# Performance work log

Measured on AMD Instinct MI355X. Metric: run time of the kernel, lower is better.

## Reference

```python
import jax, jax.numpy as jnp
import numpy as np

N, E, IN_CH, HIDDEN, N_CLASS, LAYERS = 2048, 1024, 512, 512, 40, 10
EPS = 1e-10


def setup_inputs() -> dict:
    key = jax.random.key(0)
    ks = jax.random.split(key, 6)
    x = jax.random.normal(ks[0], (1, N, IN_CH), jnp.float32)
    H = (jax.random.uniform(ks[1], (N, E)) < 0.02).astype(jnp.float32)
    # symmetric Laplacian-like operator so eigh is meaningful
    M = jax.random.normal(ks[2], (1, N, N), jnp.float32) / np.sqrt(N).astype(np.float32)
    L = 0.5 * (M + jnp.swapaxes(M, 1, 2))
    W_first = jax.random.normal(ks[3], (HIDDEN, IN_CH), jnp.float32) * 0.05
    W_mid = jax.random.normal(ks[4], (LAYERS - 2, HIDDEN, HIDDEN), jnp.float32) * 0.05
    W_last = jax.random.normal(ks[5], (N_CLASS, HIDDEN), jnp.float32) * 0.05
    return {"x": x, "L": L, "H": H, "W_first": W_first, "W_mid": W_mid, "W_last": W_last}


def _expanded_energy(x2d, H, d_v, d_e):
    # Vectorized form of the nested hyperedge/pair loop:
    # sum_e sum_{u<v in e} H_ue*H_ve/(d_e+eps) * ||x_u/sqrt(dv_u+eps) - x_v/sqrt(dv_v+eps)||^2
    # = sum_e (s_e * q_e - ||m_e||^2) / (d_e + eps)  with binary H (w_e = 1)
    y = x2d / jnp.sqrt(d_v + EPS)[:, None]          # [N, F]
    q = H.T @ jnp.sum(y * y, axis=1)                # [E] sum_u H_ue ||y_u||^2
    m = H.T @ y                                     # [E, F]
    s = jnp.sum(H, axis=0)                          # [E] edge degrees (= d_e)
    return jnp.sum((s * q - jnp.sum(m * m, axis=1)) / (d_e + EPS))


def reference(x, L, H, W_first, W_mid, W_last):
    weights = [W_first] + [W_mid[i] for i in range(LAYERS - 2)] + [W_last]
    d_v = jnp.sum(H, axis=1)
    d_e = jnp.sum(H, axis=0)
    # eigh of L is identical every layer in the original; compute once
    eigvals = jnp.linalg.eigh(L)[0]                 # [B, N]
    spectral_gap = jnp.min(jnp.where(eigvals > 1e-10, eigvals, jnp.inf))
    energies, energies_exp, snorms = [], [], []
    for i, W in enumerate(weights):
        x = jax.nn.relu(jnp.einsum('bnm,bmf->bnf', L, x) @ W.T)
        xs, Ls = x[0], L[0]                         # @torch.no_grad() blocks
        energies.append(jnp.trace(xs.T @ (Ls @ xs)))
        energies_exp.append(_expanded_energy(xs, H, d_v, d_e))
        snorms.append(jnp.linalg.norm(W, ord=2))
        # dropout skipped (eval-mode reference)
    log_probs = jax.nn.log_softmax(x, axis=1)       # dim=1 as in original
    return (log_probs, jnp.stack(energies), jnp.stack(energies_exp),
            jnp.stack(snorms), spectral_gap)
```

## Files before the change

kernel.cpp:

```cpp
#include <hip/hip_runtime.h>
#include <math.h>


typedef __attribute__((ext_vector_type(8))) short short8;
typedef __attribute__((ext_vector_type(4))) float f32x4;

#define NSHIFT 256

__device__ inline ushort bf16_rne(float f) {
    unsigned int u = __float_as_uint(f);
    return (ushort)((u + 0x7FFFu + ((u >> 16) & 1u)) >> 16);
}
__device__ inline float bf16_tof(ushort h) {
    return __uint_as_float(((unsigned int)h) << 16);
}

__device__ __forceinline__ void pbar(int* bar, int e, int w, int nwg) {
    __syncthreads();
    if (threadIdx.x == 0) {
        __threadfence();
        __hip_atomic_store(bar + 16 + w*16, e, __ATOMIC_RELAXED, __HIP_MEMORY_SCOPE_AGENT);
    }
    if (w == 0) {
        if ((int)threadIdx.x < nwg) {
            while (__hip_atomic_load(bar + 16 + threadIdx.x*16, __ATOMIC_RELAXED,
                                     __HIP_MEMORY_SCOPE_AGENT) < e)
                __builtin_amdgcn_s_sleep(1);
        }
        __syncthreads();
        if (threadIdx.x == 0)
            __hip_atomic_store(bar, e, __ATOMIC_RELEASE, __HIP_MEMORY_SCOPE_AGENT);
    } else {
        if (threadIdx.x == 0) {
            while (__hip_atomic_load(bar, __ATOMIC_RELAXED, __HIP_MEMORY_SCOPE_AGENT) < e)
                __builtin_amdgcn_s_sleep(8);
        }
    }
    if (threadIdx.x == 0) __threadfence();
    __syncthreads();
}

__global__ void init_misc(int* bar) {
    for (int j = blockIdx.x*256 + threadIdx.x; j < 16384; j += gridDim.x*256) bar[j] = 0;
}

template<bool TA, bool TB>
__device__ __forceinline__
void tile64g(const float* __restrict__ A, int lda,
             const float* __restrict__ B, int ldb,
             int bm, int bn, int k0, int k1, float acc[4][4],
             float (*sA)[68], float (*sB)[68])
{
    const int tid = threadIdx.x;
    const int tx = tid & 15, ty = tid >> 4;
    for (int kk = k0; kk < k1; kk += 16) {
        __syncthreads();
        for (int i = tid; i < 1024; i += 256) {
            int m, k2;
            if (TA) { m = i & 63; k2 = i >> 6; } else { k2 = i & 15; m = i >> 4; }
            sA[k2][m] = TA ? A[(size_t)(kk + k2)*lda + bm + m]
                           : A[(size_t)(bm + m)*lda + kk + k2];
        }
        for (int i = tid; i < 1024; i += 256) {
            int n, k2;
            if (TB) { k2 = i & 15; n = i >> 4; } else { n = i & 63; k2 = i >> 6; }
            sB[k2][n] = TB ? B[(size_t)(bn + n)*ldb + kk + k2]
                           : B[(size_t)(kk + k2)*ldb + bn + n];
        }
        __syncthreads();
        #pragma unroll
        for (int k2 = 0; k2 < 16; ++k2) {
            float4 a4 = *(const float4*)&sA[k2][ty*4];
            float4 b4 = *(const float4*)&sB[k2][tx*4];
            float av[4] = {a4.x, a4.y, a4.z, a4.w};
            float bv[4] = {b4.x, b4.y, b4.z, b4.w};
            #pragma unroll
            for (int i2 = 0; i2 < 4; ++i2)
                #pragma unroll
                for (int j2 = 0; j2 < 4; ++j2)
                    acc[i2][j2] += av[i2] * bv[j2];
        }
    }
}

template<bool TA, bool TB>
__device__ __forceinline__
void tile64d(const float* __restrict__ A, int lda,
             const float* __restrict__ B, int ldb,
             int bm, int bn, int k0, int k1, float acc[4][4],
             float (*sA)[16][68], float (*sB)[16][68])
{
    const int tid = threadIdx.x;
    const int tx = tid & 15, ty = tid >> 4;
    float ra[4], rb[4];
    auto ldregs = [&](int kk) {
        #pragma unroll
        for (int q = 0; q < 4; ++q) {
            int i = tid + q*256;
            if (TA) { int m = i & 63, k2 = i >> 6; ra[q] = A[(size_t)(kk + k2)*lda + bm + m]; }
            else    { int k2 = i & 15, m = i >> 4; ra[q] = A[(size_t)(bm + m)*lda + kk + k2]; }
            if (TB) { int k3 = i & 15, n = i >> 4; rb[q] = B[(size_t)(bn + n)*ldb + kk + k3]; }
            else    { int k3 = i >> 6, n = i & 63; rb[q] = B[(size_t)(kk + k3)*ldb + bn + n]; }
        }
    };
    auto stlds = [&](int buf) {
        #pragma unroll
        for (int q = 0; q < 4; ++q) {
            int i = tid + q*256;
            if (TA) { int m = i & 63, k2 = i >> 6; sA[buf][k2][m] = ra[q]; }
            else    { int k2 = i & 15, m = i >> 4; sA[buf][k2][m] = ra[q]; }
            if (TB) { int k3 = i & 15, n = i >> 4; sB[buf][k3][n] = rb[q]; }
            else    { int k3 = i >> 6, n = i & 63; sB[buf][k3][n] = rb[q]; }
        }
    };
    const int nit = (k1 - k0) >> 4;
    ldregs(k0);
    stlds(0);
    for (int it = 0; it < nit; ++it) {
        const int buf = it & 1;
        if (it + 1 < nit) ldregs(k0 + (it + 1)*16);
        __syncthreads();
        #pragma unroll
        for (int k2 = 0; k2 < 16; ++k2) {
            float4 a4 = *(const float4*)&sA[buf][k2][ty*4];
            float4 b4 = *(const float4*)&sB[buf][k2][tx*4];
            float av[4] = {a4.x, a4.y, a4.z, a4.w};
            float bv[4] = {b4.x, b4.y, b4.z, b4.w};
            #pragma unroll
            for (int i2 = 0; i2 < 4; ++i2)
                #pragma unroll
                for (int j2 = 0; j2 < 4; ++j2)
                    acc[i2][j2] += av[i2] * bv[j2];
        }
        if (it + 1 < nit) { __syncthreads(); stlds(buf ^ 1); }
    }
}

__device__ __forceinline__ void store_tile(float* C, int ldc, int bm, float acc[4][4]) {
    int tx = threadIdx.x & 15, ty = threadIdx.x >> 4;
    #pragma unroll
    for (int i = 0; i < 4; ++i)
        #pragma unroll
        for (int j = 0; j < 4; ++j)
            C[(size_t)(bm + ty*4 + i)*ldc + tx*4 + j] = acc[i][j];
}

__global__ void init_q0(float* Q) {
    int idx = blockIdx.x*256 + threadIdx.x;
    if (idx < 2048*64) {
        int n = idx >> 6, c = idx & 63;
        Q[(size_t)n*2048 + c] = (n == c) ? 1.f : 0.f;
    }
}

__global__ __launch_bounds__(256)
void lz_LQ(const float* __restrict__ Lm, const float* __restrict__ Qs, float* __restrict__ Cp)
{
    __shared__ float sA[2][16][68], sB[2][16][68];
    int z = blockIdx.x, mt = blockIdx.y;
    float acc[4][4] = {};
    tile64d<false,false>(Lm, 2048, Qs, 2048, mt*64, 0, z*256, z*256 + 256, acc, sA, sB);
    store_tile(Cp + (size_t)z*131072, 64, mt*64, acc);
}

__global__ void lz_sumZ(const float* __restrict__ Cp, float* __restrict__ Z)
{
    int idx = blockIdx.x*256 + threadIdx.x;
    float v = 0.f;
    #pragma unroll
    for (int z = 0; z < 8; ++z) v += Cp[(size_t)z*131072 + idx];
    Z[idx] = v;
}

__global__ __launch_bounds__(256)
void lz_QTZ(const float* __restrict__ Qall, const float* __restrict__ Z, float* __restrict__ Cp)
{
    __shared__ float sA[2][16][68], sB[2][16][68];
    int z = blockIdx.x, b = blockIdx.y;
    float acc[4][4] = {};
    tile64d<true,false>(Qall, 2048, Z, 64, b*64, 0, z*256, z*256 + 256, acc, sA, sB);
    store_tile(Cp + (size_t)z*131072, 64, b*64, acc);
}

__global__ void lz_sumC(const float* __restrict__ Cp, float* __restrict__ Creo,
                        float* __restrict__ Ab, int s)
{
    int idx = blockIdx.x*256 + threadIdx.x;
    float v = 0.f;
    #pragma unroll
    for (int z = 0; z < 8; ++z) v += Cp[(size_t)z*131072 + idx];
    Creo[idx] = v;
    if ((idx >> 6) >= 64*s) Ab[(size_t)s*4096 + (idx - s*4096)] = v;
}

__global__ __launch_bounds__(256)
void lz_QC(const float* __restrict__ Qall, const float* __restrict__ Creo,
           float* __restrict__ Cp, int s)
{
    __shared__ float sA[2][16][68], sB[2][16][68];
    int z = blockIdx.x, mt = blockIdx.y;
    float acc[4][4] = {};
    for (int j = z; j <= s; j += 8)
        tile64d<false,false>(Qall, 2048, Creo, 64, mt*64, 0, j*64, j*64 + 64, acc, sA, sB);
    store_tile(Cp + (size_t)z*131072, 64, mt*64, acc);
}

__global__ __launch_bounds__(256)
void lz_finZ(float* __restrict__ Z, const float* __restrict__ Cp, int nz,
             double* __restrict__ Gp)
{
    __shared__ float zb[64][65];
    int w = blockIdx.x, tid = threadIdx.x;
    for (int idx = tid; idx < 4096; idx += 256) {
        size_t o = (size_t)w*4096 + idx;
        float v = Z[o];
        for (int z = 0; z < nz; ++z) v -= Cp[(size_t)z*131072 + o];
        Z[o] = v;
        zb[idx >> 6][idx & 63] = v;
    }
    __syncthreads();
    int tx = tid & 15, ty = tid >> 4;
    double acc[4][4] = {};
    for (int r = 0; r < 64; ++r) {
        float av[4], bv[4];
        #pragma unroll
        for (int q = 0; q < 4; ++q) { av[q] = zb[r][ty*4 + q]; bv[q] = zb[r][tx*4 + q]; }
        #pragma unroll
        for (int i = 0; i < 4; ++i)
            #pragma unroll
            for (int j = 0; j < 4; ++j)
                acc[i][j] += (double)av[i] * (double)bv[j];
    }
    #pragma unroll
    for (int i = 0; i < 4; ++i)
        #pragma unroll
        for (int j = 0; j < 4; ++j)
            Gp[(size_t)w*4096 + (size_t)(ty*4 + i)*64 + tx*4 + j] = acc[i][j];
}

__global__ __launch_bounds__(256)
void lz_chol(const double* __restrict__ Gp, float* __restrict__ RinvF, float* __restrict__ BbS)
{
    __shared__ double G[64][65];
    __shared__ double Xs[64][65];
    __shared__ double lv[64];
    int tid = threadIdx.x;
    for (int idx = tid; idx < 4096; idx += 256) {
        double g = 0.0;
        for (int z = 0; z < 32; ++z) g += Gp[(size_t)z*4096 + idx];
        G[idx>>6][idx&63] = g;
    }
    __syncthreads();
    for (int k = 0; k < 64; ++k) {
        if (tid < 64) {
            double rkk = sqrt(fmax(G[k][k], 1e-40));
            lv[tid] = (tid == k) ? rkk : ((tid > k) ? G[k][tid]/rkk : 0.0);
        }
        __syncthreads();
        if (tid < 64 && tid >= k) G[k][tid] = lv[tid];
        for (int idx = tid; idx < 4096; idx += 256) {
            int i = idx>>6, j = idx&63;
            if (i > k && j >= i) G[i][j] -= lv[i]*lv[j];
        }
        __syncthreads();
    }
    for (int idx = tid; idx < 4096; idx += 256) {
        int i = idx>>6, j = idx&63;
        BbS[idx] = (j >= i) ? (float)G[i][j] : 0.f;
        Xs[i][j] = 0.0;
    }
    __syncthreads();
    if (tid < 64) {
        int j = tid;
        for (int i = j; i >= 0; --i) {
            double s2 = (i == j) ? 1.0 : 0.0;
            for (int k2 = i + 1; k2 <= j; ++k2) s2 -= G[i][k2]*Xs[k2][j];
            Xs[i][j] = s2 / G[i][i];
        }
    }
    __syncthreads();
    for (int idx = tid; idx < 4096; idx += 256)
        RinvF[idx] = (float)Xs[idx>>6][idx&63];
}

__global__ __launch_bounds__(256)
void lz_apply(const float* __restrict__ Z, const float* __restrict__ Rinv, float* __restrict__ Qn)
{
    __shared__ float sA[2][16][68], sB[2][16][68];
    int w = blockIdx.x;
    float acc[4][4] = {};
    tile64d<false,false>(Z, 64, Rinv, 64, w*64, 0, 0, 64, acc, sA, sB);
    store_tile(Qn, 2048, w*64, acc);
}

__global__ void assemble_band(const float* Ab, const float* Bb, float* band) {
    int idx = blockIdx.x*256 + threadIdx.x;
    if (idx >= 2048*65) return;
    int c = idx / 65, r = idx % 65;
    int row = c + r;
    float v = 0.f;
    if (row < 2048) {
        int j = c >> 6, q = c & 63, rr = q + r;
        if (rr <= 63) {
            const float* A = Ab + (size_t)j*4096;
            v = 0.5f*(A[rr*64 + q] + A[q*64 + rr]);
        } else if (j < 31) {
            int p = rr - 64;
            v = Bb[(size_t)j*4096 + p*64 + q];
        }
    }
    band[idx] = v;
}

__device__ __forceinline__
void pack_item(int idx, const float* __restrict__ src, const float* __restrict__ dv,
               ushort* __restrict__ Bh, ushort* __restrict__ Bl,
               ushort* __restrict__ Ch, ushort* __restrict__ Cl)
{
    int l = idx & 63, t = idx >> 6;
    int nb = t & 31, kc = t >> 5;
    int col = nb*16 + (l & 15);
    int k0 = kc*32 + ((l >> 4) << 3);
    ushort h8[8], l8[8], sh8[8], sl8[8];
    #pragma unroll
    for (int j = 0; j < 8; ++j) {
        int k = k0 + j;
        float v = src[(size_t)k*512 + col];
        ushort hb = bf16_rne(v);
        h8[j] = hb; l8[j] = bf16_rne(v - bf16_tof(hb));
        if (Ch) {
            float t2 = v * (1.0f / sqrtf(dv[k] + 1e-10f));
            ushort hb2 = bf16_rne(t2);
            sh8[j] = hb2; sl8[j] = bf16_rne(t2 - bf16_tof(hb2));
        }
    }
    uint4 hv, lv;
    hv.x = (unsigned)h8[0] | ((unsigned)h8[1] << 16);
    hv.y = (unsigned)h8[2] | ((unsigned)h8[3] << 16);
    hv.z = (unsigned)h8[4] | ((unsigned)h8[5] << 16);
    hv.w = (unsigned)h8[6] | ((unsigned)h8[7] << 16);
    lv.x = (unsigned)l8[0] | ((unsigned)l8[1] << 16);
    lv.y = (unsigned)l8[2] | ((unsigned)l8[3] << 16);
    lv.z = (unsigned)l8[4] | ((unsigned)l8[5] << 16);
    lv.w = (unsigned)l8[6] | ((unsigned)l8[7] << 16);
    *(uint4*)(Bh + (size_t)idx*8) = hv;
    *(uint4*)(Bl + (size_t)idx*8) = lv;
    if (Ch) {
        uint4 shv, slv;
        shv.x = (unsigned)sh8[0] | ((unsigned)sh8[1] << 16);
        shv.y = (unsigned)sh8[2] | ((unsigned)sh8[3] << 16);
        shv.z = (unsigned)sh8[4] | ((unsigned)sh8[5] << 16);
        shv.w = (unsigned)sh8[6] | ((unsigned)sh8[7] << 16);
        slv.x = (unsigned)sl8[0] | ((unsigned)sl8[1] << 16);
        slv.y = (unsigned)sl8[2] | ((unsigned)sl8[3] << 16);
        slv.z = (unsigned)sl8[4] | ((unsigned)sl8[5] << 16);
        slv.w = (unsigned)sl8[6] | ((unsigned)sl8[7] << 16);
        *(uint4*)(Ch + (size_t)idx*8) = shv;
        *(uint4*)(Cl + (size_t)idx*8) = slv;
    }
}

__global__ void pack_both(const float* __restrict__ src, const float* __restrict__ dv,
                          ushort* __restrict__ Bh, ushort* __restrict__ Bl,
                          ushort* __restrict__ Ch, ushort* __restrict__ Cl)
{
    int idx = blockIdx.x*256 + threadIdx.x;
    if (idx < 131072) pack_item(idx, src, dv, Bh, Bl, Ch, Cl);
}

__global__ void pack_A_L(const float* __restrict__ src, int Kld, int MB,
                         ushort* __restrict__ Ah, ushort* __restrict__ Al, int total)
{
    int idx = blockIdx.x*256 + threadIdx.x;
    if (idx >= total) return;
    int l = idx & 63, t = idx >> 6;
    int mb = t % MB, kc = t / MB;
    int m = mb*16 + (l & 15);
    int k0 = kc*32 + ((l >> 4) << 3);
    const float* p = src + (size_t)m*Kld + k0;
    float4 a = *(const float4*)p, b = *(const float4*)(p + 4);
    float vv[8] = {a.x,a.y,a.z,a.w,b.x,b.y,b.z,b.w};
    ushort h8[8], l8[8];
    #pragma unroll
    for (int j = 0; j < 8; ++j) {
        ushort hb = bf16_rne(vv[j]);
        h8[j] = hb; l8[j] = bf16_rne(vv[j] - bf16_tof(hb));
    }
    uint4 hv, lv;
    hv.x = (unsigned)h8[0] | ((unsigned)h8[1] << 16);
    hv.y = (unsigned)h8[2] | ((unsigned)h8[3] << 16);
    hv.z = (unsigned)h8[4] | ((unsigned)h8[5] << 16);
    hv.w = (unsigned)h8[6] | ((unsigned)h8[7] << 16);
    lv.x = (unsigned)l8[0] | ((unsigned)l8[1] << 16);
    lv.y = (unsigned)l8[2] | ((unsigned)l8[3] << 16);
    lv.z = (unsigned)l8[4] | ((unsigned)l8[5] << 16);
    lv.w = (unsigned)l8[6] | ((unsigned)l8[7] << 16);
    *(uint4*)(Ah + (size_t)idx*8) = hv;
    *(uint4*)(Al + (size_t)idx*8) = lv;
}

__global__ void pack_A_T(const float* __restrict__ src, int Mld, int MB,
                         ushort* __restrict__ Ah, int total)
{
    int idx = blockIdx.x*256 + threadIdx.x;
    if (idx >= total) return;
    int l = idx & 63, t = idx >> 6;
    int mb = t % MB, kc = t / MB;
    int m = mb*16 + (l & 15);
    int k0 = kc*32 + ((l >> 4) << 3);
    ushort h8[8];
    #pragma unroll
    for (int j = 0; j < 8; ++j)
        h8[j] = bf16_rne(src[(size_t)(k0 + j)*Mld + m]);
    uint4 hv;
    hv.x = (unsigned)h8[0] | ((unsigned)h8[1] << 16);
    hv.y = (unsigned)h8[2] | ((unsigned)h8[3] << 16);
    hv.z = (unsigned)h8[4] | ((unsigned)h8[5] << 16);
    hv.w = (unsigned)h8[6] | ((unsigned)h8[7] << 16);
    *(uint4*)(Ah + (size_t)idx*8) = hv;
}

__device__ __forceinline__
void mfma_task(int t, const ushort* __restrict__ Lph, const ushort* __restrict__ Lpl,
               const ushort* __restrict__ Bh, const ushort* __restrict__ Bl,
               const ushort* __restrict__ Htp,
               const ushort* __restrict__ Bqh, const ushort* __restrict__ Bql,
               float* __restrict__ U, float* __restrict__ ME,
               ushort (*lA)[4096], ushort (*lB)[4096])
{
    const bool isU = (t < 64);
    const ushort* Ah = isU ? Lph : Htp;
    const ushort* Al = isU ? Lpl : nullptr;
    const ushort* Xh = isU ? Bh : Bqh;
    const ushort* Xl = isU ? Bl : Bql;
    float* C = isU ? U : ME;
    const int MB = isU ? 128 : 64;
    const int tmb = (isU ? (t >> 2) : ((t - 64) >> 2)) * 8;
    const int tnb = (t & 3) * 8;
    const int KC = 64;
    const int tid = threadIdx.x;
    const int lane = tid & 63, wave = tid >> 6;
    const int wr = wave >> 1, wc = wave & 1;

    f32x4 acc[4][4];
    #pragma unroll
    for (int i = 0; i < 4; ++i)
        #pragma unroll
        for (int j = 0; j < 4; ++j) acc[i][j] = (f32x4){0.f,0.f,0.f,0.f};

    uint4 rAh[2], rAl[2], rBh[2], rBl[2];
    auto loadregs = [&](int kc) {
        const uint4* pa = (const uint4*)(Ah + ((size_t)kc*MB + tmb)*512);
        rAh[0] = pa[tid]; rAh[1] = pa[tid + 256];
        if (Al) {
            const uint4* pl = (const uint4*)(Al + ((size_t)kc*MB + tmb)*512);
            rAl[0] = pl[tid]; rAl[1] = pl[tid + 256];
        }
        const uint4* pb = (const uint4*)(Xh + ((size_t)kc*32 + tnb)*512);
        rBh[0] = pb[tid]; rBh[1] = pb[tid + 256];
        const uint4* pc = (const uint4*)(Xl + ((size_t)kc*32 + tnb)*512);
        rBl[0] = pc[tid]; rBl[1] = pc[tid + 256];
    };

    loadregs(0);
    for (int kc = 0; kc < KC; ++kc) {
        __syncthreads();
        *(uint4*)&lA[0][tid*8]       = rAh[0];
        *(uint4*)&lA[0][(tid+256)*8] = rAh[1];
        if (Al) {
            *(uint4*)&lA[1][tid*8]       = rAl[0];
            *(uint4*)&lA[1][(tid+256)*8] = rAl[1];
        }
        *(uint4*)&lB[0][tid*8]       = rBh[0];
        *(uint4*)&lB[0][(tid+256)*8] = rBh[1];
        *(uint4*)&lB[1][tid*8]       = rBl[0];
        *(uint4*)&lB[1][(tid+256)*8] = rBl[1];
        if (kc + 1 < KC) loadregs(kc + 1);
        __syncthreads();

        short8 a_h[4], a_l[4], b_h[4], b_l[4];
        #pragma unroll
        for (int i = 0; i < 4; ++i) {
            a_h[i] = *(const short8*)&lA[0][(((wr*4 + i)*64) + lane)*8];
            if (Al) a_l[i] = *(const short8*)&lA[1][(((wr*4 + i)*64) + lane)*8];
        }
        #pragma unroll
        for (int j = 0; j < 4; ++j) {
            b_h[j] = *(const short8*)&lB[0][(((wc*4 + j)*64) + lane)*8];
            b_l[j] = *(const short8*)&lB[1][(((wc*4 + j)*64) + lane)*8];
        }
        #pragma unroll
        for (int i = 0; i < 4; ++i)
            #pragma unroll
            for (int j = 0; j < 4; ++j) {
                acc[i][j] = __builtin_amdgcn_mfma_f32_16x16x32_bf16(a_h[i], b_h[j], acc[i][j], 0, 0, 0);
                acc[i][j] = __builtin_amdgcn_mfma_f32_16x16x32_bf16(a_h[i], b_l[j], acc[i][j], 0, 0, 0);
                if (Al)
                    acc[i][j] = __builtin_amdgcn_mfma_f32_16x16x32_bf16(a_l[i], b_h[j], acc[i][j], 0, 0, 0);
            }
    }
    const int r0 = tmb*16 + wr*64, c0 = tnb*16 + wc*64;
    #pragma unroll
    for (int i = 0; i < 4; ++i)
        #pragma unroll
        for (int j = 0; j < 4; ++j) {
            int row = r0 + i*16 + ((lane >> 4) << 2);
            int col = c0 + j*16 + (lane & 15);
            #pragma unroll
            for (int r = 0; r < 4; ++r)
                C[(size_t)(row + r)*512 + col] = acc[i][j][r];
        }
}

__global__ __launch_bounds__(256, 2)
void mgemm_dual(const ushort* __restrict__ Lph, const ushort* __restrict__ Lpl,
                const ushort* __restrict__ Bh, const ushort* __restrict__ Bl,
                const ushort* __restrict__ Htp,
                const ushort* __restrict__ Bqh, const ushort* __restrict__ Bql,
                float* __restrict__ U, float* __restrict__ ME)
{
    __shared__ ushort lA[2][4096];
    __shared__ ushort lB[2][4096];
    int t = blockIdx.y * 4 + blockIdx.x;
    mfma_task(t, Lph, Lpl, Bh, Bl, Htp, Bqh, Bql, U, ME, lA, lB);
}

__global__ __launch_bounds__(256, 1)
void mlp_persist(float* __restrict__ u, float* __restrict__ h,
                 const float* __restrict__ Wf, const float* __restrict__ Wm,
                 const ushort* __restrict__ Lph, const ushort* __restrict__ Lpl,
                 const ushort* __restrict__ Htp,
                 ushort* __restrict__ bpkh, ushort* __restrict__ bpkl,
                 ushort* __restrict__ bqh, ushort* __restrict__ bql,
                 const float* __restrict__ H, const float* __restrict__ dv,
                 const float* __restrict__ de,
                 float* __restrict__ mEb, float* __restrict__ srowp,
                 float* __restrict__ qpart,
                 float* __restrict__ parts512, float* __restrict__ parts16,
                 float* __restrict__ outp, int* __restrict__ bar)
{
    const int w = blockIdx.x, tid = threadIdx.x;
    __shared__ char smem[35072];
    __shared__ float red4[4];
    __shared__ float sRs[64];
    float (*sA)[68] = (float(*)[68])smem;
    float (*sB)[68] = (float(*)[68])(smem + 4352);
    float (*sT)[65] = (float(*)[65])smem;
    ushort (*lA)[4096] = (ushort(*)[4096])smem;
    ushort (*lB)[4096] = (ushort(*)[4096])(smem + 16384);
    int ep = 0;
    const int mt = w >> 3, nt = w & 7;
    const int tx = tid & 15, ty = tid >> 4;

    for (int k = 0; k < 9; ++k) {
        const float* W = (k == 0) ? Wf : Wm + (size_t)(k-1)*262144;
        if (w == 0 && k > 0 && tid < 64) {
            float s = parts512[tid] + parts512[tid+64] + parts512[tid+128] + parts512[tid+192];
            for (int o = 32; o; o >>= 1) s += __shfl_down(s, o, 64);
            float x = (tid < 16) ? parts16[tid] : 0.f;
            for (int o = 32; o; o >>= 1) x += __shfl_down(x, o, 64);
            if (tid == 0) { outp[81920 + k - 1] = s; outp[81930 + k - 1] = x; }
        }
        {
            float acc[4][4] = {};
            tile64g<false,true>(u, 512, W, 512, mt*64, nt*64, 0, 512, acc, sA, sB);
            __syncthreads();
            if (tid < 64) sRs[tid] = 1.0f / sqrtf(dv[mt*64 + tid] + 1e-10f);
            #pragma unroll
            for (int i = 0; i < 4; ++i)
                #pragma unroll
                for (int j = 0; j < 4; ++j) {
                    float v = fmaxf(acc[i][j], 0.f);
                    h[(size_t)(mt*64 + ty*4 + i)*512 + nt*64 + tx*4 + j] = v;
                    sT[ty*4 + i][tx*4 + j] = v;
                }
            __syncthreads();
            #pragma unroll
            for (int q = 0; q < 2; ++q) {
                int it = tid + q*256;
                int a = it >> 8, rem = it & 255;
                int b = rem >> 6, lane = rem & 63;
                int cl = b*16 + (lane & 15);
                int r0 = a*32 + ((lane >> 4) << 3);
                int idxg = (((2*mt + a)*32 + (4*nt + b))*64 + lane);
                ushort h8[8], l8[8], sh8[8], sl8[8];
                #pragma unroll
                for (int j = 0; j < 8; ++j) {
                    float v = sT[r0 + j][cl];
                    ushort hb = bf16_rne(v);
                    h8[j] = hb; l8[j] = bf16_rne(v - bf16_tof(hb));
                    float t2 = v * sRs[r0 + j];
                    ushort hb2 = bf16_rne(t2);
                    sh8[j] = hb2; sl8[j] = bf16_rne(t2 - bf16_tof(hb2));
                }
                uint4 hv, lv, shv, slv;
                hv.x = (unsigned)h8[0] | ((unsigned)h8[1] << 16);
                hv.y = (unsigned)h8[2] | ((unsigned)h8[3] << 16);
                hv.z = (unsigned)h8[4] | ((unsigned)h8[5] << 16);
                hv.w = (unsigned)h8[6] | ((unsigned)h8[7] << 16);
                lv.x = (unsigned)l8[0] | ((unsigned)l8[1] << 16);
                lv.y = (unsigned)l8[2] | ((unsigned)l8[3] << 16);
                lv.z = (unsigned)l8[4] | ((unsigned)l8[5] << 16);
                lv.w = (unsigned)l8[6] | ((unsigned)l8[7] << 16);
                shv.x = (unsigned)sh8[0] | ((unsigned)sh8[1] << 16);
                shv.y = (unsigned)sh8[2] | ((unsigned)sh8[3] << 16);
                shv.z = (unsigned)sh8[4] | ((unsigned)sh8[5] << 16);
                shv.w = (unsigned)sh8[6] | ((unsigned)sh8[7] << 16);
                slv.x = (unsigned)sl8[0] | ((unsigned)sl8[1] << 16);
                slv.y = (unsigned)sl8[2] | ((unsigned)sl8[3] << 16);
                slv.z = (unsigned)sl8[4] | ((unsigned)sl8[5] << 16);
                slv.w = (unsigned)sl8[6] | ((unsigned)sl8[7] << 16);
                *(uint4*)(bpkh + (size_t)idxg*8) = hv;
                *(uint4*)(bpkl + (size_t)idxg*8) = lv;
                *(uint4*)(bqh  + (size_t)idxg*8) = shv;
                *(uint4*)(bql  + (size_t)idxg*8) = slv;
            }
            if (tid < 64) {
                float rs = sRs[tid];
                float ss = 0.f;
                for (int c = 0; c < 64; ++c) { float v = sT[tid][c]; ss += v*v; }
                srowp[(size_t)nt*2048 + mt*64 + tid] = ss * rs * rs;
            }
        }
        pbar(bar, ++ep, w, 256);
        if (w < 96) {
            mfma_task(w, Lph, Lpl, bpkh, bpkl, Htp, bqh, bql, u, mEb, lA, lB);
        } else if (w < 128) {
            int task = w - 96;
            int e = (task & 3)*256 + tid;
            int zc = task >> 2;
            float s = 0.f;
            for (int n = zc*256; n < zc*256 + 256; ++n) {
                float sr = 0.f;
                #pragma unroll
                for (int p2 = 0; p2 < 8; ++p2) sr += srowp[(size_t)p2*2048 + n];
                s += H[(size_t)n*1024 + e] * sr;
            }
            qpart[(size_t)zc*1024 + e] = s;
        }
        pbar(bar, ++ep, w, 256);
        if (w < 16) {
            int wave = tid >> 6, lane = tid & 63;
            float acc = 0.f;
            for (int t2 = 0; t2 < 16; ++t2) {
                int e = w*64 + wave*16 + t2;
                float me2 = 0.f;
                for (int f = lane; f < 512; f += 64) { float v = mEb[(size_t)e*512 + f]; me2 += v*v; }
                for (int o = 32; o; o >>= 1) me2 += __shfl_down(me2, o, 64);
                if (lane == 0) {
                    float q = 0.f;
                    for (int z = 0; z < 8; ++z) q += qpart[(size_t)z*1024 + e];
                    acc += (de[e]*q - me2) / (de[e] + 1e-10f);
                }
            }
            if (lane == 0) red4[wave] = acc;
            __syncthreads();
            if (tid == 0) parts16[w] = red4[0]+red4[1]+red4[2]+red4[3];
            __syncthreads();
        }
        {
            int lane = tid & 63;
            float dd = 0.f;
            #pragma unroll
            for (int g = 0; g < 2; ++g) {
                int row = w*8 + g*4 + (tid >> 6);
                for (int f = lane; f < 512; f += 64)
                    dd += h[(size_t)row*512 + f] * u[(size_t)row*512 + f];
            }
            for (int o = 32; o; o >>= 1) dd += __shfl_down(dd, o, 64);
            __syncthreads();
            if (lane == 0) red4[tid >> 6] = dd;
            __syncthreads();
            if (tid == 0) parts512[w] = red4[0]+red4[1]+red4[2]+red4[3];
        }
        pbar(bar, ++ep, w, 256);
    }
    if (w == 0 && tid < 64) {
        float s = parts512[tid] + parts512[tid+64] + parts512[tid+128] + parts512[tid+192];
        for (int o = 32; o; o >>= 1) s += __shfl_down(s, o, 64);
        float x = (tid < 16) ? parts16[tid] : 0.f;
        for (int o = 32; o; o >>= 1) x += __shfl_down(x, o, 64);
        if (tid == 0) { outp[81928] = s; outp[81938] = x; }
    }
}

template<bool TA, bool TB>
__global__ __launch_bounds__(256)
void gemm_f32(const float* A, int lda, const float* B, int ldb,
              float* C, int ldc, float* Cpart,
              int M, int N, int K, float alpha, float beta, int relu)
{
    const int S = (int)gridDim.z, z = (int)blockIdx.z;
    const int kchunk = (K + S - 1) / S;
    const int k0 = z * kchunk;
    const int k1 = (K < k0 + kchunk) ? K : (k0 + kchunk);
    const int bm = blockIdx.y * 64, bn = blockIdx.x * 64;
    __shared__ float As[16][68];
    __shared__ float Bs[16][68];
    const int tid = threadIdx.x;
    const int tx = tid & 15, ty = tid >> 4;
    float acc[4][4] = {};
    for (int kk = k0; kk < k1; kk += 16) {
        for (int i = tid; i < 1024; i += 256) {
            int m, k;
            if (TA) { m = i & 63; k = i >> 6; } else { k = i & 15; m = i >> 4; }
            int gm = bm + m, gk = kk + k;
            float v = 0.f;
            if (gm < M && gk < k1) v = TA ? A[(size_t)gk*lda + gm] : A[(size_t)gm*lda + gk];
            As[k][m] = v;
        }
        for (int i = tid; i < 1024; i += 256) {
            int n, k;
            if (TB) { k = i & 15; n = i >> 4; } else { n = i & 63; k = i >> 6; }
            int gn = bn + n, gk = kk + k;
            float v = 0.f;
            if (gn < N && gk < k1) v = TB ? B[(size_t)gn*ldb + gk] : B[(size_t)gk*ldb + gn];
            Bs[k][n] = v;
        }
        __syncthreads();
        #pragma unroll
        for (int k = 0; k < 16; ++k) {
            float4 ra4 = *reinterpret_cast<const float4*>(&As[k][ty*4]);
            float4 rb4 = *reinterpret_cast<const float4*>(&Bs[k][tx*4]);
            float ra[4] = {ra4.x, ra4.y, ra4.z, ra4.w};
            float rb[4] = {rb4.x, rb4.y, rb4.z, rb4.w};
            #pragma unroll
            for (int i = 0; i < 4; ++i)
                #pragma unroll
                for (int j = 0; j < 4; ++j)
                    acc[i][j] += ra[i] * rb[j];
        }
        __syncthreads();
    }
    if (S == 1) {
        #pragma unroll
        for (int i = 0; i < 4; ++i) {
            int gm = bm + ty*4 + i;
            if (gm >= M) continue;
            #pragma unroll
            for (int j = 0; j < 4; ++j) {
                int gn = bn + tx*4 + j;
                if (gn >= N) continue;
                float v = alpha * acc[i][j];
                if (beta != 0.f) v += beta * C[(size_t)gm*ldc + gn];
                if (relu) v = fmaxf(v, 0.f);
                C[(size_t)gm*ldc + gn] = v;
            }
        }
    } else {
        float* P = Cpart + (size_t)z * M * N;
        #pragma unroll
        for (int i = 0; i < 4; ++i) {
            int gm = bm + ty*4 + i;
            if (gm >= M) continue;
            #pragma unroll
            for (int j = 0; j < 4; ++j) {
                int gn = bn + tx*4 + j;
                if (gn >= N) continue;
                P[(size_t)gm*N + gn] = alpha * acc[i][j];
            }
        }
    }
}

__global__ void reduce_parts(const float* Cpart, float* C, int M, int N, int ldc,
                             int S, float beta, int relu)
{
    int total = M * N;
    for (int idx = blockIdx.x*256 + threadIdx.x; idx < total; idx += gridDim.x*256) {
        float s = 0.f;
        for (int z = 0; z < S; ++z) s += Cpart[(size_t)z*total + idx];
        int mm = idx / N, nn = idx % N;
        float v = s;
        if (beta != 0.f) v += beta * C[(size_t)mm*ldc + nn];
        if (relu) v = fmaxf(v, 0.f);
        C[(size_t)mm*ldc + nn] = v;
    }
}

__global__ void row_deg(const float* H, float* dv) {
    int row = blockIdx.x*4 + (threadIdx.x >> 6);
    int lane = threadIdx.x & 63;
    if (row >= 2048) return;
    float s = 0.f;
    for (int e = lane; e < 1024; e += 64) s += H[(size_t)row*1024 + e];
    for (int o = 32; o; o >>= 1) s += __shfl_down(s, o, 64);
    if (lane == 0) dv[row] = s;
}

__global__ void coldot_part(const float* H, const float* w, float* part) {
    int e = blockIdx.x*256 + threadIdx.x;
    int zc = blockIdx.y;
    float s = 0.f;
    if (w) {
        for (int n = zc*256; n < zc*256 + 256; ++n) s += H[(size_t)n*1024 + e] * w[n];
    } else {
        for (int n = zc*256; n < zc*256 + 256; ++n) s += H[(size_t)n*1024 + e];
    }
    part[(size_t)zc*1024 + e] = s;
}
__global__ void coldot_fin(const float* part, float* outp) {
    int e = blockIdx.x*256 + threadIdx.x;
    float s = 0.f;
    for (int z = 0; z < 8; ++z) s += part[(size_t)z*1024 + e];
    outp[e] = s;
}

__global__ void dotsrow(const float* h, const float* u, int F, const float* dv,
                        float* srow, float* yout, float* parts)
{
    int row = blockIdx.x*4 + (threadIdx.x >> 6);
    int lane = threadIdx.x & 63;
    __shared__ float a4[4];
    float rs = 1.0f / sqrtf(dv[row] + 1e-10f);
    float ss = 0.f, dd = 0.f;
    for (int f = lane; f < F; f += 64) {
        float hv = h[(size_t)row*F + f];
        float t = hv * rs;
        if (yout) yout[(size_t)row*F + f] = t;
        ss += t*t;
        dd += hv * u[(size_t)row*F + f];
    }
    for (int o = 32; o; o >>= 1) { ss += __shfl_down(ss, o, 64); dd += __shfl_down(dd, o, 64); }
    if (lane == 0) { srow[row] = ss; a4[threadIdx.x >> 6] = dd; }
    __syncthreads();
    if (threadIdx.x == 0) parts[blockIdx.x] = a4[0]+a4[1]+a4[2]+a4[3];
}

__global__ void edge_energy(const float* m, int F, const float* de, const float* qpart,
                            float* partials) {
    int wave = threadIdx.x >> 6, lane = threadIdx.x & 63;
    __shared__ float acc4[4];
    float acc = 0.f;
    for (int t = 0; t < 16; ++t) {
        int e = blockIdx.x*64 + wave*16 + t;
        float me2 = 0.f;
        for (int f = lane; f < F; f += 64) { float v = m[(size_t)e*F + f]; me2 += v*v; }
        for (int o = 32; o; o >>= 1) me2 += __shfl_down(me2, o, 64);
        if (lane == 0) {
            float q = 0.f;
            for (int z = 0; z < 8; ++z) q += qpart[(size_t)z*1024 + e];
            acc += (de[e]*q - me2) / (de[e] + 1e-10f);
        }
    }
    if (lane == 0) acc4[wave] = acc;
    __syncthreads();
    if (threadIdx.x == 0) partials[blockIdx.x] = acc4[0]+acc4[1]+acc4[2]+acc4[3];
}

__global__ void finalize2(const float* p512, const float* p16, float* oe, float* ox) {
    __shared__ float red[256];
    int tid = threadIdx.x;
    red[tid] = p512[tid] + p512[tid + 256];
    __syncthreads();
    for (int st = 128; st; st >>= 1) { if (tid < st) red[tid] += red[tid+st]; __syncthreads(); }
    if (tid == 0) *oe = red[0];
    __syncthreads();
    red[tid] = (tid < 16) ? p16[tid] : 0.f;
    __syncthreads();
    for (int st = 128; st; st >>= 1) { if (tid < st) red[tid] += red[tid+st]; __syncthreads(); }
    if (tid == 0) *ox = red[0];
}

__global__ void logsoftmax(const float* xf, float* outp) {
    __shared__ float red[256];
    int c = blockIdx.x, tid = threadIdx.x;
    float mx = -3.0e38f;
    for (int n = tid; n < 2048; n += 256) mx = fmaxf(mx, xf[(size_t)n*40 + c]);
    red[tid] = mx; __syncthreads();
    for (int st = 128; st; st >>= 1) { if (tid < st) red[tid] = fmaxf(red[tid], red[tid+st]); __syncthreads(); }
    mx = red[0]; __syncthreads();
    float s = 0.f;
    for (int n = tid; n < 2048; n += 256) s += expf(xf[(size_t)n*40 + c] - mx);
    red[tid] = s; __syncthreads();
    for (int st = 128; st; st >>= 1) { if (tid < st) red[tid] += red[tid+st]; __syncthreads(); }
    float lse = mx + logf(red[0]);
    for (int n = tid; n < 2048; n += 256) outp[(size_t)n*40 + c] = xf[(size_t)n*40 + c] - lse;
}

__global__ __launch_bounds__(256)
void band_count(const float* __restrict__ band, const double* __restrict__ shifts,
                int* __restrict__ counts)
{
    __shared__ double win[66][66];
    const int tid = threadIdx.x;
    const double sigma = shifts[blockIdx.x];
    int ei[9], ej[9];
    {
        int i = 1, S = 0;
        #pragma unroll
        for (int k = 0; k < 9; ++k) {
            int T = tid + k*256;
            if (T < 2080) {
                while (S + (65 - i) <= T) { S += 65 - i; ++i; }
                ei[k] = i; ej[k] = i + (T - S);
            } else { ei[k] = 0; ej[k] = 0; }
        }
    }
    for (int idx = tid; idx < 65*65; idx += 256) {
        int c0 = idx / 65, r = idx % 65;
        win[c0][r] = (double)band[c0*65 + r] - (r == 0 ? sigma : 0.0);
    }
    __syncthreads();
    int cnt = 0;
    for (int c = 0; c < 2048; ++c) {
        const int p = c % 66;
        double d = win[p][0];
        if (fabs(d) < 1e-100) d = (d < 0 ? -1e-100 : 1e-100);
        if (d < 0) cnt++;
        double inv = 1.0 / d;
        #pragma unroll
        for (int k = 0; k < 9; ++k) {
            int i = ei[k];
            if (i) {
                int j = ej[k];
                int r2 = p + i; if (r2 >= 66) r2 -= 66;
                win[r2][j - i] -= win[p][i] * inv * win[p][j];
            }
        }
        int cn = c + 65;
        int slot = p + 65; if (slot >= 66) slot -= 66;
        if (tid < 65)
            win[slot][tid] = (cn < 2048)
                ? ((double)band[(size_t)cn*65 + tid] - (tid == 0 ? sigma : 0.0)) : 0.0;
        __syncthreads();
    }
    if (tid == 0) counts[blockIdx.x] = cnt;
}

__global__ void bisect(double* shifts, const int* counts, double* st, float* gap_out, int mode) {
    if (threadIdx.x != 0) return;
    if (mode == 0) {
        shifts[0] = 1e-10;
        double l0 = log(1e-6), l1 = log(0.5);
        for (int i = 1; i < NSHIFT; ++i) shifts[i] = exp(l0 + (l1 - l0)*(i - 1)/(double)(NSHIFT - 2));
        return;
    }
    if (mode == 1) {
        int n0 = counts[0];
        double lo = shifts[NSHIFT-1], hi = 1.5;
        for (int i = 1; i < NSHIFT; ++i) if (counts[i] > n0) { lo = shifts[i-1]; hi = shifts[i]; break; }
        st[0] = lo; st[1] = hi; st[2] = (double)n0;
        for (int i = 0; i < NSHIFT; ++i) shifts[i] = lo + (hi - lo)*(i + 1)/(double)(NSHIFT + 1);
        return;
    }
    int n0 = (int)st[2];
    double lo = st[0], hi = st[1];
    double nlo = shifts[NSHIFT-1], nhi = hi;
    for (int i = 0; i < NSHIFT; ++i) if (counts[i] > n0) { nhi = shifts[i]; nlo = (i == 0) ? lo : shifts[i-1]; break; }
    *gap_out = (float)(0.5*(nlo + nhi));
}

__global__ __launch_bounds__(256)
void gram9(const float* __restrict__ Wf, const float* __restrict__ Wm, float* __restrict__ sG)
{
    int mi = blockIdx.z;
    const float* W = (mi == 0) ? Wf : Wm + (size_t)(mi-1)*262144;
    __shared__ float sA[16][68], sB[16][68];
    int tid = threadIdx.x, tx = tid & 15, ty = tid >> 4;
    int bm = blockIdx.y*64, bn = blockIdx.x*64;
    float acc[4][4] = {};
    for (int kk = 0; kk < 512; kk += 16) {
        __syncthreads();
        for (int i = tid; i < 1024; i += 256) { int m = i&63, k = i>>6; sA[k][m] = W[(size_t)(kk+k)*512 + bm+m]; }
        for (int i = tid; i < 1024; i += 256) { int n = i&63, k = i>>6; sB[k][n] = W[(size_t)(kk+k)*512 + bn+n]; }
        __syncthreads();
        #pragma unroll
        for (int k = 0; k < 16; ++k) {
            float4 a4 = *(const float4*)&sA[k][ty*4];
            float4 b4 = *(const float4*)&sB[k][tx*4];
            float av[4]={a4.x,a4.y,a4.z,a4.w}, bv[4]={b4.x,b4.y,b4.z,b4.w};
            #pragma unroll
            for (int i = 0; i < 4; ++i)
                #pragma unroll
                for (int j = 0; j < 4; ++j) acc[i][j] += av[i]*bv[j];
        }
    }
    float* C = sG + (size_t)mi*262144;
    #pragma unroll
    for (int i = 0; i < 4; ++i)
        #pragma unroll
        for (int j = 0; j < 4; ++j)
            C[(size_t)(bm + ty*4 + i)*512 + bn + tx*4 + j] = acc[i][j];
}

__global__ __launch_bounds__(256)
void snorm_lanczos(const float* Gall, const float* Wl, float* outp) {
    int w = blockIdx.x, tid = threadIdx.x;
    int n = (w < 9) ? 512 : 40;
    const float* G = Gall + (size_t)w*262144;
    __shared__ float g40[1600];
    __shared__ float v[512], vp[512], wv[512], red[256];
    __shared__ float al[32], be[32];
    if (w == 9) {
        for (int p = tid; p < 1600; p += 256) {
            int i = p / 40, j = p % 40;
            float s = 0.f;
            for (int k2 = 0; k2 < 512; ++k2) s += Wl[(size_t)i*512 + k2]*Wl[(size_t)j*512 + k2];
            g40[p] = s;
        }
        __syncthreads();
    }
    float inv0 = 1.f / sqrtf((float)n);
    for (int i = tid; i < n; i += 256) { v[i] = inv0; vp[i] = 0.f; }
    __syncthreads();
    float beta_prev = 0.f;
    for (int s = 0; s < 32; ++s) {
        for (int r = tid; r < n; r += 256) {
            float sum = 0.f;
            if (w < 9) { const float* row = G + (size_t)r*512; for (int k2 = 0; k2 < 512; ++k2) sum += row[k2]*v[k2]; }
            else       { const float* row = &g40[r*40];        for (int k2 = 0; k2 < 40;  ++k2) sum += row[k2]*v[k2]; }
            wv[r] = sum;
        }
        __syncthreads();
        float p = 0.f;
        for (int i = tid; i < n; i += 256) p += v[i]*wv[i];
        red[tid] = p; __syncthreads();
        for (int st = 128; st; st >>= 1) { if (tid < st) red[tid] += red[tid+st]; __syncthreads(); }
        float alpha = red[0]; __syncthreads();
        for (int i = tid; i < n; i += 256) wv[i] -= alpha*v[i] + beta_prev*vp[i];
        __syncthreads();
        p = 0.f;
        for (int i = tid; i < n; i += 256) p += wv[i]*wv[i];
        red[tid] = p; __syncthreads();
        for (int st = 128; st; st >>= 1) { if (tid < st) red[tid] += red[tid+st]; __syncthreads(); }
        float beta = sqrtf(fmaxf(red[0], 0.f)); __syncthreads();
        if (tid == 0) { al[s] = alpha; be[s] = beta; }
        float ib = 1.f / fmaxf(beta, 1e-20f);
        for (int i = tid; i < n; i += 256) { float t = v[i]; vp[i] = t; v[i] = wv[i]*ib; }
        beta_prev = beta;
        __syncthreads();
    }
    if (tid == 0) {
        float hi = 0.f;
        for (int s = 0; s < 32; ++s) {
            float g2 = al[s] + be[s] + (s ? be[s-1] : 0.f);
            hi = fmaxf(hi, g2);
        }
        float lo = 0.f;
        for (int it = 0; it < 48; ++it) {
            float mid = 0.5f*(lo + hi);
            float d = al[0] - mid; int c2 = (d < 0.f);
            for (int s = 1; s < 32; ++s) {
                float dp = d;
                if (fabsf(dp) < 1e-25f) dp = (dp < 0.f) ? -1e-25f : 1e-25f;
                d = (al[s] - mid) - be[s-1]*be[s-1]/dp;
                c2 += (d < 0.f);
            }
            if (c2 == 32) hi = mid; else lo = mid;
        }
        outp[w] = sqrtf(fmaxf(0.5f*(lo + hi), 0.f));
    }
}

static void gemm64(hipStream_t st, int ta, int tb, int M, int N, int K,
                   const float* A, int lda, const float* B, int ldb,
                   float* C, int ldc, float alpha, float beta, int relu,
                   float* Cpart, int S)
{
    dim3 grid((unsigned)((N + 63)/64), (unsigned)((M + 63)/64), (unsigned)S);
    if (!ta && !tb)      gemm_f32<false,false><<<grid,256,0,st>>>(A,lda,B,ldb,C,ldc,Cpart,M,N,K,alpha,beta,relu);
    else if (!ta && tb)  gemm_f32<false,true ><<<grid,256,0,st>>>(A,lda,B,ldb,C,ldc,Cpart,M,N,K,alpha,beta,relu);
    else if (ta && !tb)  gemm_f32<true ,false><<<grid,256,0,st>>>(A,lda,B,ldb,C,ldc,Cpart,M,N,K,alpha,beta,relu);
    else                 gemm_f32<true ,true ><<<grid,256,0,st>>>(A,lda,B,ldb,C,ldc,Cpart,M,N,K,alpha,beta,relu);
    if (S > 1) {
        int total = M * N;
        int g = (total + 255)/256; if (g > 2048) g = 2048;
        reduce_parts<<<g,256,0,st>>>(Cpart, C, M, N, ldc, S, beta, relu);
    }
}

extern "C" void kernel_launch(void* const* d_in, const int* in_sizes, int n_in,
                              void* d_out, int out_size, void* d_ws, size_t ws_size,
                              hipStream_t stream)
{
    (void)in_sizes; (void)n_in; (void)out_size; (void)ws_size;
    const float* X  = (const float*)d_in[0];
    const float* Lm = (const float*)d_in[1];
    const float* H  = (const float*)d_in[2];
    const float* Wf = (const float*)d_in[3];
    const float* Wm = (const float*)d_in[4];
    const float* Wl = (const float*)d_in[5];
    float* out = (float*)d_out;

    float* ws = (float*)d_ws;
    size_t off = 0;
    auto alloc = [&](size_t n) { float* p = ws + off; off += (n + 255) & ~(size_t)255; return p; };
    float* Lph_f  = alloc((size_t)2097152);
    float* Lpl_f  = alloc((size_t)2097152);
    float* Htp_f  = alloc((size_t)1048576);
    float* bpkh_f = alloc((size_t)524288);
    float* bpkl_f = alloc((size_t)524288);
    float* h      = alloc((size_t)2048*512);
    float* u      = alloc((size_t)2048*512);
    float* mEb    = alloc((size_t)1024*512);
    float* Cpart  = alloc((size_t)1024*1024);
    float* srowp  = alloc((size_t)8*2048);
    float* dv     = alloc(2048);
    float* de     = alloc(1024);
    float* srow   = alloc(2048);
    float* qpart  = alloc(8*1024);
    float* parts512 = alloc(512);
    float* parts16  = alloc(256);
    double* shifts  = (double*)alloc(2*NSHIFT);
    double* bstate  = (double*)alloc(8);
    int* counts     = (int*)alloc(NSHIFT);
    int* barbase    = (int*)alloc(16384);

    ushort* Lph  = (ushort*)Lph_f;
    ushort* Lpl  = (ushort*)Lpl_f;
    ushort* Htp  = (ushort*)Htp_f;
    ushort* bpkh = (ushort*)bpkh_f;
    ushort* bpkl = (ushort*)bpkl_f;
    ushort* bqh  = (ushort*)Cpart;
    ushort* bql  = (ushort*)(Cpart + 524288);
    int* barM = barbase;
    float* Qall  = Lph_f;
    float* Z     = Htp_f;
    float* Creo  = Htp_f + 131072;
    float* Ab    = Htp_f + 262144;
    float* Bb    = Htp_f + 393216;
    float* band  = Htp_f + 524288;
    float* Rinv  = Htp_f + 658432;
    double* GpD  = (double*)bpkh_f;
    float* sG    = Qall;
    float* h9  = mEb;
    float* y9  = mEb + 131072;
    float* mE9 = mEb + 262144;

    init_misc<<<16,256,0,stream>>>(barbase);
    pack_A_L<<<2048,256,0,stream>>>(Lm, 2048, 128, Lph, Lpl, 524288);
    pack_A_T<<<1024,256,0,stream>>>(H, 1024, 64, Htp, 262144);
    row_deg<<<512,256,0,stream>>>(H, dv);
    coldot_part<<<dim3(4,8),256,0,stream>>>(H, nullptr, qpart);
    coldot_fin<<<4,256,0,stream>>>(qpart, de);

    pack_both<<<512,256,0,stream>>>(X, dv, bpkh, bpkl, nullptr, nullptr);
    mgemm_dual<<<dim3(4,16),256,0,stream>>>(Lph, Lpl, bpkh, bpkl, Htp, bqh, bql, u, mEb);

    mlp_persist<<<256,256,0,stream>>>(u, h, Wf, Wm, Lph, Lpl, Htp,
                                      bpkh, bpkl, bqh, bql, H, dv, de,
                                      mEb, srowp, qpart, parts512, parts16, out, barM);

    gemm64(stream, 0,1, 2048,40,512, u,512, Wl,512, h9,40, 1.f,0.f,1, Cpart,8);
    gemm64(stream, 0,0, 2048,40,2048, Lm,2048, h9,40, u,40, 1.f,0.f,0, Cpart,8);
    dotsrow<<<512,256,0,stream>>>(h9, u, 40, dv, srow, y9, parts512);
    coldot_part<<<dim3(4,8),256,0,stream>>>(H, srow, qpart);
    gemm64(stream, 1,0, 1024,40,2048, H,1024, y9,40, mE9,40, 1.f,0.f,0, Cpart,8);
    edge_energy<<<16,256,0,stream>>>(mE9, 40, de, qpart, parts16);
    finalize2<<<1,256,0,stream>>>(parts512, parts16, out + 81929, out + 81939);
    logsoftmax<<<40,256,0,stream>>>(h9, out);

    init_q0<<<512,256,0,stream>>>(Qall);
    for (int s = 0; s < 32; ++s) {
        lz_LQ<<<dim3(8,32),256,0,stream>>>(Lm, Qall + 64*s, Cpart);
        lz_sumZ<<<512,256,0,stream>>>(Cpart, Z);
        lz_QTZ<<<dim3(8,(unsigned)(s+1)),256,0,stream>>>(Qall, Z, Cpart);
        lz_sumC<<<(s+1)*16,256,0,stream>>>(Cpart, Creo, Ab, s);
        if (s == 31) break;
        int nz = (s + 1 < 8) ? s + 1 : 8;
        lz_QC<<<dim3((unsigned)nz,32),256,0,stream>>>(Qall, Creo, Cpart, s);
        lz_finZ<<<32,256,0,stream>>>(Z, Cpart, nz, GpD);
        lz_chol<<<1,256,0,stream>>>(GpD, Rinv, Bb + (size_t)s*4096);
        lz_apply<<<32,256,0,stream>>>(Z, Rinv, Qall + (size_t)64*(s+1));
    }
    assemble_band<<<520,256,0,stream>>>(Ab, Bb, band);

    bisect<<<1,64,0,stream>>>(shifts, counts, bstate, out + 81950, 0);
    band_count<<<NSHIFT,256,0,stream>>>(band, shifts, counts);
    bisect<<<1,64,0,stream>>>(shifts, counts, bstate, out + 81950, 1);
    band_count<<<NSHIFT,256,0,stream>>>(band, shifts, counts);
    bisect<<<1,64,0,stream>>>(shifts, counts, bstate, out + 81950, 3);

    gram9<<<dim3(8,8,9),256,0,stream>>>(Wf, Wm, sG);
    snorm_lanczos<<<10,256,0,stream>>>(sG, Wl, out + 81940);
}
```

Before: 15.37 ms.

## Fuse Lanczos finZ, Cholesky and apply kernels using grid barriers

Merges the three per-iteration block-Lanczos tail kernels (Z update with partial Gram, single-block Cholesky/inverse, Q = Z·Rinv) into one persistent 32-block kernel. The stages are separated by device-wide software barriers instead of kernel launches, and shared memory is reused across phases through one aliased buffer. The aim is to cut two launches and their gaps per iteration across 31 iterations. In exchange, 31 blocks spin while block 0 does the serial Cholesky, and correctness depends on all 32 blocks being co-resident.

```diff
diff --git a/kernel.cpp b/kernel.cpp
--- a/kernel.cpp
+++ b/kernel.cpp
@@ -205,12 +205,21 @@
     store_tile(Cp + (size_t)z*131072, 64, mt*64, acc);
 }
 
-__global__ __launch_bounds__(256)
-void lz_finZ(float* __restrict__ Z, const float* __restrict__ Cp, int nz,
-             double* __restrict__ Gp)
-{
-    __shared__ float zb[64][65];
-    int w = blockIdx.x, tid = threadIdx.x;
+__global__ __launch_bounds__(256, 1)
+void lz_tail(float* __restrict__ Z, const float* __restrict__ Cp, int nz,
+             double* __restrict__ Gp, float* __restrict__ RinvF,
+             float* __restrict__ BbS, float* __restrict__ Qn,
+             int* __restrict__ bar, int ep0)
+{
+    const int w = blockIdx.x, tid = threadIdx.x;
+    __shared__ char smem[67072];
+    float (*zb)[65]  = (float(*)[65])smem;
+    double (*G)[65]  = (double(*)[65])smem;
+    double (*Xs)[65] = (double(*)[65])(smem + 33280);
+    double* lv       = (double*)(smem + 66560);
+    float (*sA)[16][68] = (float(*)[16][68])smem;
+    float (*sB)[16][68] = (float(*)[16][68])(smem + 8704);
+
     for (int idx = tid; idx < 4096; idx += 256) {
         size_t o = (size_t)w*4096 + idx;
         float v = Z[o];
@@ -219,78 +228,72 @@
         zb[idx >> 6][idx & 63] = v;
     }
     __syncthreads();
-    int tx = tid & 15, ty = tid >> 4;
-    double acc[4][4] = {};
-    for (int r = 0; r < 64; ++r) {
-        float av[4], bv[4];
-        #pragma unroll
-        for (int q = 0; q < 4; ++q) { av[q] = zb[r][ty*4 + q]; bv[q] = zb[r][tx*4 + q]; }
+    {
+        int tx = tid & 15, ty = tid >> 4;
+        double acc[4][4] = {};
+        for (int r = 0; r < 64; ++r) {
+            float av[4], bv[4];
+            #pragma unroll
+            for (int q = 0; q < 4; ++q) { av[q] = zb[r][ty*4 + q]; bv[q] = zb[r][tx*4 + q]; }
+            #pragma unroll
+            for (int i = 0; i < 4; ++i)
+                #pragma unroll
+                for (int j = 0; j < 4; ++j)
+                    acc[i][j] += (double)av[i] * (double)bv[j];
+        }
         #pragma unroll
         for (int i = 0; i < 4; ++i)
             #pragma unroll
             for (int j = 0; j < 4; ++j)
-                acc[i][j] += (double)av[i] * (double)bv[j];
-    }
-    #pragma unroll
-    for (int i = 0; i < 4; ++i)
-        #pragma unroll
-        for (int j = 0; j < 4; ++j)
-            Gp[(size_t)w*4096 + (size_t)(ty*4 + i)*64 + tx*4 + j] = acc[i][j];
-}
-
-__global__ __launch_bounds__(256)
-void lz_chol(const double* __restrict__ Gp, float* __restrict__ RinvF, float* __restrict__ BbS)
-{
-    __shared__ double G[64][65];
-    __shared__ double Xs[64][65];
-    __shared__ double lv[64];
-    int tid = threadIdx.x;
-    for (int idx = tid; idx < 4096; idx += 256) {
-        double g = 0.0;
-        for (int z = 0; z < 32; ++z) g += Gp[(size_t)z*4096 + idx];
-        G[idx>>6][idx&63] = g;
-    }
-    __syncthreads();
-    for (int k = 0; k < 64; ++k) {
-        if (tid < 64) {
-            double rkk = sqrt(fmax(G[k][k], 1e-40));
-            lv[tid] = (tid == k) ? rkk : ((tid > k) ? G[k][tid]/rkk : 0.0);
-        }
-        __syncthreads();
-        if (tid < 64 && tid >= k) G[k][tid] = lv[tid];
+                Gp[(size_t)w*4096 + (size_t)(ty*4 + i)*64 + tx*4 + j] = acc[i][j];
+    }
+    pbar(bar, ep0, w, 32);
+
+    if (w == 0) {
+        for (int idx = tid; idx < 4096; idx += 256) {
+            double g = 0.0;
+            for (int z = 0; z < 32; ++z) g += Gp[(size_t)z*4096 + idx];
+            G[idx>>6][idx&63] = g;
+        }
+        __syncthreads();
+        for (int k = 0; k < 64; ++k) {
+            if (tid < 64) {
+                double rkk = sqrt(fmax(G[k][k], 1e-40));
+                lv[tid] = (tid == k) ? rkk : ((tid > k) ? G[k][tid]/rkk : 0.0);
+            }
+            __syncthreads();
+            if (tid < 64 && tid >= k) G[k][tid] = lv[tid];
+            for (int idx = tid; idx < 4096; idx += 256) {
+                int i = idx>>6, j = idx&63;
+                if (i > k && j >= i) G[i][j] -= lv[i]*lv[j];
+            }
+            __syncthreads();
+        }
         for (int idx = tid; idx < 4096; idx += 256) {
             int i = idx>>6, j = idx&63;
-            if (i > k && j >= i) G[i][j] -= lv[i]*lv[j];
-        }
-        __syncthreads();
-    }
-    for (int idx = tid; idx < 4096; idx += 256) {
-        int i = idx>>6, j = idx&63;
-        BbS[idx] = (j >= i) ? (float)G[i][j] : 0.f;
-        Xs[i][j] = 0.0;
-    }
-    __syncthreads();
-    if (tid < 64) {
-        int j = tid;
-        for (int i = j; i >= 0; --i) {
-            double s2 = (i == j) ? 1.0 : 0.0;
-            for (int k2 = i + 1; k2 <= j; ++k2) s2 -= G[i][k2]*Xs[k2][j];
-            Xs[i][j] = s2 / G[i][i];
-        }
-    }
-    __syncthreads();
-    for (int idx = tid; idx < 4096; idx += 256)
-        RinvF[idx] = (float)Xs[idx>>6][idx&63];
-}
-
-__global__ __launch_bounds__(256)
-void lz_apply(const float* __restrict__ Z, const float* __restrict__ Rinv, float* __restrict__ Qn)
-{
-    __shared__ float sA[2][16][68], sB[2][16][68];
-    int w = blockIdx.x;
-    float acc[4][4] = {};
-    tile64d<false,false>(Z, 64, Rinv, 64, w*64, 0, 0, 64, acc, sA, sB);
-    store_tile(Qn, 2048, w*64, acc);
+            BbS[idx] = (j >= i) ? (float)G[i][j] : 0.f;
+            Xs[i][j] = 0.0;
+        }
+        __syncthreads();
+        if (tid < 64) {
+            int j = tid;
+            for (int i = j; i >= 0; --i) {
+                double s2 = (i == j) ? 1.0 : 0.0;
+                for (int k2 = i + 1; k2 <= j; ++k2) s2 -= G[i][k2]*Xs[k2][j];
+                Xs[i][j] = s2 / G[i][i];
+            }
+        }
+        __syncthreads();
+        for (int idx = tid; idx < 4096; idx += 256)
+            RinvF[idx] = (float)Xs[idx>>6][idx&63];
+    }
+    pbar(bar, ep0 + 1, w, 32);
+
+    {
+        float acc[4][4] = {};
+        tile64d<false,false>(Z, 64, RinvF, 64, w*64, 0, 0, 64, acc, sA, sB);
+        store_tile(Qn, 2048, w*64, acc);
+    }
 }
 
 __global__ void assemble_band(const float* Ab, const float* Bb, float* band) {
@@ -1115,6 +1118,7 @@
     ushort* bqh  = (ushort*)Cpart;
     ushort* bql  = (ushort*)(Cpart + 524288);
     int* barM = barbase;
+    int* barL = barbase + 8192;
     float* Qall  = Lph_f;
     float* Z     = Htp_f;
     float* Creo  = Htp_f + 131072;
@@ -1160,9 +1164,9 @@
         if (s == 31) break;
         int nz = (s + 1 < 8) ? s + 1 : 8;
         lz_QC<<<dim3((unsigned)nz,32),256,0,stream>>>(Qall, Creo, Cpart, s);
-        lz_finZ<<<32,256,0,stream>>>(Z, Cpart, nz, GpD);
-        lz_chol<<<1,256,0,stream>>>(GpD, Rinv, Bb + (size_t)s*4096);
-        lz_apply<<<32,256,0,stream>>>(Z, Rinv, Qall + (size_t)64*(s+1));
+        lz_tail<<<32,256,0,stream>>>(Z, Cpart, nz, GpD, Rinv,
+                                     Bb + (size_t)s*4096, Qall + (size_t)64*(s+1),
+                                     barL, 2*s + 1);
     }
     assemble_band<<<520,256,0,stream>>>(Ab, Bb, band);
 
```

New measurement: 15.39 ms. No clear change (+0.1%).
